# Kernel tuning notes

Measured on AMD Instinct MI355X. Metric: run time of the kernel, lower is better.

Reference implementation:

```python
import jax, jax.numpy as jnp
import numpy as np
from jax import lax

B, T, CIN, COUT, FACTOR = 2, 2048, 512, 512, 2
KUP = FACTOR * 2          # transposed-conv kernel
PUP = FACTOR // 2         # transposed-conv padding
KR, PR = 7, 3             # refine conv kernel/padding
EPS = 1e-5


def _ste(x, q):
    # straight-through estimator: forward = q, backward = identity
    return x + lax.stop_gradient(q - x)


def act_quant(x):
    # BitNet b1.58 per-token int8 absmax quant; x is (B, C, L), quant over C
    scale = 127.0 / jnp.maximum(jnp.max(jnp.abs(x), axis=1, keepdims=True), 1e-5)
    q = jnp.clip(jnp.round(x * scale), -128, 127) / scale
    return _ste(x, q)


def weight_quant(w):
    # ternary {-1,0,1} * scale, scale = mean |w|
    scale = 1.0 / jnp.maximum(jnp.mean(jnp.abs(w)), 1e-5)
    q = jnp.clip(jnp.round(w * scale), -1, 1) / scale
    return _ste(w, q)


def bit_conv1d(x, w, b, pad):
    # x: (B,C,L), w: (Cout,Cin,K) torch layout
    y = lax.conv_general_dilated(
        act_quant(x), weight_quant(w), window_strides=(1,),
        padding=[(pad, pad)], dimension_numbers=('NCH', 'OIH', 'NCH'))
    return y + b[None, :, None]


def bit_conv_transpose1d(x, w, b, stride, pad):
    # x: (B,Cin,L), w: (Cin,Cout,K) torch ConvTranspose1d layout
    k = w.shape[2]
    y = lax.conv_general_dilated(
        act_quant(x), jnp.flip(weight_quant(w), 2), window_strides=(1,),
        padding=[(k - 1 - pad, k - 1 - pad)], lhs_dilation=(stride,),
        dimension_numbers=('NCH', 'IOH', 'NCH'))
    return y + b[None, :, None]


def setup_inputs() -> dict:
    key = jax.random.key(0)
    ks = jax.random.split(key, 7)
    s_up = 1.0 / np.sqrt(CIN * KUP)
    s_r = 1.0 / np.sqrt(COUT * KR)
    return {
        'x': jax.random.normal(ks[0], (B, T, CIN), jnp.float32),
        'w_up': jax.random.normal(ks[1], (CIN, COUT, KUP), jnp.float32) * s_up,
        'b_up': jnp.zeros((COUT,), jnp.float32),
        'w_r1': jax.random.normal(ks[2], (COUT, COUT, KR), jnp.float32) * s_r,
        'b_r1': jnp.zeros((COUT,), jnp.float32),
        'w_r2': jax.random.normal(ks[3], (COUT, COUT, KR), jnp.float32) * s_r,
        'b_r2': jnp.zeros((COUT,), jnp.float32),
        'ln_w': jnp.ones((COUT,), jnp.float32),
        'ln_b': jnp.zeros((COUT,), jnp.float32),
    }


def reference(x, w_up, b_up, w_r1, b_r1, w_r2, b_r2, ln_w, ln_b):
    h = jnp.swapaxes(x, 1, 2)                                  # (B,Cin,T)
    h = bit_conv_transpose1d(h, w_up, b_up, FACTOR, PUP)       # (B,Cout,factor*T)
    r = bit_conv1d(h, w_r1, b_r1, PR)
    r = jax.nn.silu(r)
    r = bit_conv1d(r, w_r2, b_r2, PR)
    h = h + r
    h = jnp.swapaxes(h, 1, 2)                                  # (B,L,Cout)
    mu = jnp.mean(h, axis=-1, keepdims=True)
    var = jnp.mean(jnp.square(h - mu), axis=-1, keepdims=True)
    return (h - mu) * lax.rsqrt(var + EPS) * ln_w + ln_b
```

## Files before the change

kernel.cpp:

```cpp
#include <hip/hip_runtime.h>
#include <hip/hip_bf16.h>
#include <cstdint>
#include <cstddef>


#define B_ 2
#define T_ 2048
#define L_ 4096
#define C_ 512

static constexpr int NUP = 512 * 512 * 4;
static constexpr int NR  = 512 * 512 * 7;

using v4i  = __attribute__((ext_vector_type(4))) int;
using v16i = __attribute__((ext_vector_type(16))) int;

__device__ __forceinline__ void gl16(const void* g, void* l) {
  __builtin_amdgcn_global_load_lds((const __attribute__((address_space(1))) unsigned int*)g,
                                   (__attribute__((address_space(3))) unsigned int*)l,
                                   16, 0, 0);
}


__device__ inline float block_reduce_sum_256(float v) {
  #pragma unroll
  for (int off = 32; off > 0; off >>= 1) v += __shfl_down(v, off, 64);
  __shared__ float s[4];
  __syncthreads();
  if ((threadIdx.x & 63) == 0) s[threadIdx.x >> 6] = v;
  __syncthreads();
  return (s[0] + s[1]) + (s[2] + s[3]);
}

__global__ void abssum3_partial(const float* __restrict__ w0, const float* __restrict__ w1,
                                const float* __restrict__ w2, float* __restrict__ partial) {
  int y = blockIdx.y;
  const float* w = (y == 0) ? w0 : (y == 1) ? w1 : w2;
  int n = (y == 0) ? NUP : NR;
  int idx = blockIdx.x * 256 + threadIdx.x;
  float s = 0.f;
  for (int i = idx; i < n; i += gridDim.x * 256) s += fabsf(w[i]);
  s = block_reduce_sum_256(s);
  if (threadIdx.x == 0) partial[y * 256 + blockIdx.x] = s;
}

__global__ void abssum3_final(const float* __restrict__ partial, float* __restrict__ out) {
  int y = blockIdx.x;
  float v = partial[y * 256 + threadIdx.x];
  v = block_reduce_sum_256(v);
  if (threadIdx.x == 0) out[y] = v;
}

__global__ void tern_all_kernel(const float* __restrict__ wu, const float* __restrict__ w1,
                                const float* __restrict__ w2, int8_t* __restrict__ ou,
                                int8_t* __restrict__ o1, int8_t* __restrict__ o2,
                                const float* __restrict__ wsum) {
  int y = blockIdx.y;
  int idx = blockIdx.x * 256 + threadIdx.x;
  if (y == 0) {
    if (idx >= NUP) return;
    float mean = wsum[0] * (1.0f / (float)NUP);
    float scale = 1.0f / fmaxf(mean, 1e-5f);
    float t = rintf(wu[idx] * scale);
    t = fminf(fmaxf(t, -1.f), 1.f);
    int ci = idx >> 11;
    int co = (idx >> 2) & 511;
    int k = idx & 3;
    int ptap = (k == 3) ? 0 : (k == 1) ? 1 : (k == 2) ? 2 : 3;
    ou[(((size_t)ptap * 32 + (ci >> 4)) * 512 + co) * 16 + (ci & 15)] = (int8_t)t;
  } else {
    if (idx >= NR) return;
    const float* w = (y == 1) ? w1 : w2;
    int8_t* o = (y == 1) ? o1 : o2;
    float mean = wsum[y] * (1.0f / (float)NR);
    float scale = 1.0f / fmaxf(mean, 1e-5f);
    float t = rintf(w[idx] * scale);
    t = fminf(fmaxf(t, -1.f), 1.f);
    int co = idx / 3584;
    int rem = idx - co * 3584;
    int ci = rem / 7;
    int k = rem - ci * 7;
    o[(((size_t)k * 32 + (ci >> 4)) * 512 + co) * 16 + (ci & 15)] = (int8_t)t;
  }
}

__global__ void act_quant_kernel(const float* __restrict__ x, int8_t* __restrict__ qd,
                                 float* __restrict__ inv, int Lb, int lbsh, int LinH) {
  int tok = blockIdx.x;
  int b = tok >> lbsh;
  int t = tok & (Lb - 1);
  const float* row = x + (size_t)tok * C_;
  int tid = threadIdx.x;
  float v0 = row[tid];
  float v1 = row[tid + 256];
  float m = fmaxf(fabsf(v0), fabsf(v1));
  #pragma unroll
  for (int off = 32; off > 0; off >>= 1) m = fmaxf(m, __shfl_down(m, off, 64));
  __shared__ float s[4];
  __shared__ __align__(16) int8_t sq[512];
  if ((tid & 63) == 0) s[tid >> 6] = m;
  __syncthreads();
  m = fmaxf(fmaxf(s[0], s[1]), fmaxf(s[2], s[3]));
  float scale = 127.0f / fmaxf(m, 1e-5f);
  float q0 = fminf(fmaxf(rintf(v0 * scale), -128.f), 127.f);
  float q1 = fminf(fmaxf(rintf(v1 * scale), -128.f), 127.f);
  sq[tid] = (int8_t)q0;
  sq[tid + 256] = (int8_t)q1;
  __syncthreads();
  if (tid < 32)
    *(v4i*)(qd + ((size_t)(b * 32 + tid) * LinH + 8 + t) * 16) = *(const v4i*)(sq + tid * 16);
  if (tid == 0) inv[(size_t)b * LinH + 8 + t] = 1.0f / scale;
}

template<int NTAPS, bool CONVT>
__global__ __launch_bounds__(512, 4)
void conv_mfma(const int8_t* __restrict__ qin, const float* __restrict__ invp, int LinH,
               const int8_t* __restrict__ wq, const float* __restrict__ wsum, int widx,
               float wninv, const float* __restrict__ bias, const float* __restrict__ res,
               float* __restrict__ outp, int Lout, int do_silu) {
  __shared__ __align__(16) int8_t sA[32 * 38 * 16];
  __shared__ float sInv[40];

  const int tid = threadIdx.x;
  const int w = tid >> 6, lane = tid & 63, q = lane >> 5, l31 = lane & 31;
  const int n0 = (blockIdx.x & 1) * 256;
  const int t0 = (blockIdx.x >> 1) * 32;
  const int b = blockIdx.y;
  int s0 = -3;
  const int8_t* wq_p = wq;
  float* out_b = outp + (size_t)b * Lout * 512;
  int rstride = 512;
  if (CONVT) {
    int parity = blockIdx.z;
    s0 = parity - 1;
    wq_p += (size_t)parity * 2 * 32 * 512 * 16;
    out_b += parity * 512;
    rstride = 1024;
  }
  const int8_t* qin_b = qin + (size_t)b * 32 * LinH * 16;
  const float* inv_b = invp + (size_t)b * LinH + 8;

  #pragma unroll
  for (int i = 0; i < 3; ++i) {
    int base = i * 512 + w * 64;
    if (base < 1216) {
      int u = base + lane;
      int kq = u / 38;
      int row = u - kq * 38;
      gl16(qin_b + ((size_t)kq * LinH + (size_t)(t0 + 5 + row)) * 16,
           sA + (size_t)base * 16);
    }
  }
  if (tid < 38) sInv[tid] = inv_b[t0 - 3 + tid];
  __syncthreads();

  float fs[16];
  v16i accA{}, accB{};
  #pragma unroll
  for (int r = 0; r < 16; ++r) { fs[r] = 0.f; accA[r] = 0; accB[r] = 0; }

  const int col = n0 + w * 32 + l31;
  const int8_t* wt_base = wq_p + ((size_t)q * 512 + (size_t)col) * 16;

  #pragma unroll 1
  for (int tap = 0; tap < NTAPS; ++tap) {
    const int shift = s0 + tap;
    const int8_t* aP = sA + (((size_t)q * 38) + (size_t)(3 + shift + l31)) * 16;
    const int8_t* wt = wt_base + (size_t)tap * (32 * 512 * 16);
    #pragma unroll
    for (int ks = 0; ks < 16; ks += 2) {
      v4i a0 = *(const v4i*)(aP + (size_t)ks * (2 * 38 * 16));
      v4i b0 = *(const v4i*)(wt + (size_t)ks * 16384);
      accA = __builtin_amdgcn_mfma_i32_32x32x32_i8(a0, b0, accA, 0, 0, 0);
      v4i a1 = *(const v4i*)(aP + (size_t)(ks + 1) * (2 * 38 * 16));
      v4i b1 = *(const v4i*)(wt + (size_t)(ks + 1) * 16384);
      accB = __builtin_amdgcn_mfma_i32_32x32x32_i8(a1, b1, accB, 0, 0, 0);
    }
    #pragma unroll
    for (int r = 0; r < 16; ++r) {
      int ro = (r & 3) + 8 * (r >> 2) + 4 * q;
      float sc = sInv[3 + shift + ro];
      fs[r] = fmaf((float)(accA[r] + accB[r]), sc, fs[r]);
      accA[r] = 0; accB[r] = 0;
    }
  }

  float wdq = fmaxf(wsum[widx] * wninv, 1e-5f);
  float bv = bias[col];
  #pragma unroll
  for (int r = 0; r < 16; ++r) {
    int row = t0 + (r & 3) + 8 * (r >> 2) + 4 * q;
    float y = fs[r] * wdq + bv;
    if (do_silu) y = y / (1.0f + expf(-y));
    if (res) y += res[((size_t)b * Lout + row) * 512 + col];
    out_b[(size_t)row * rstride + col] = y;
  }
}

__global__ void ln_kernel(const float* __restrict__ x, const float* __restrict__ g,
                          const float* __restrict__ be, float* __restrict__ out) {
  int tok = blockIdx.x;
  const float* row = x + (size_t)tok * C_;
  int tid = threadIdx.x;
  float v0 = row[tid];
  float v1 = row[tid + 256];
  float total = block_reduce_sum_256(v0 + v1);
  float mu = total * (1.0f / (float)C_);
  float d0 = v0 - mu, d1 = v1 - mu;
  float vs = block_reduce_sum_256(d0 * d0 + d1 * d1);
  float var = vs * (1.0f / (float)C_);
  float r = 1.0f / sqrtf(var + 1e-5f);
  size_t base = (size_t)tok * C_;
  out[base + tid] = d0 * r * g[tid] + be[tid];
  out[base + tid + 256] = d1 * r * g[tid + 256] + be[tid + 256];
}


extern "C" void kernel_launch(void* const* d_in, const int* in_sizes, int n_in,
                              void* d_out, int out_size, void* d_ws, size_t ws_size,
                              hipStream_t stream) {
  const float* x    = (const float*)d_in[0];
  const float* w_up = (const float*)d_in[1];
  const float* b_up = (const float*)d_in[2];
  const float* w_r1 = (const float*)d_in[3];
  const float* b_r1 = (const float*)d_in[4];
  const float* w_r2 = (const float*)d_in[5];
  const float* b_r2 = (const float*)d_in[6];
  const float* ln_w = (const float*)d_in[7];
  const float* ln_b = (const float*)d_in[8];
  float* out = (float*)d_out;

  const int LXH = T_ + 16;
  const int LHH = L_ + 16;

  char* ws = (char*)d_ws;
  size_t off = 0;
  auto alloc = [&](size_t sz) { size_t p = off; off += (sz + 255) & ~(size_t)255; return p; };
  float*  wsum = (float*) (ws + alloc(256));
  int8_t* qx   = (int8_t*)(ws + alloc((size_t)B_ * 32 * LXH * 16));
  int8_t* qh   = (int8_t*)(ws + alloc((size_t)B_ * 32 * LHH * 16));
  float*  invx = (float*) (ws + alloc((size_t)B_ * LXH * 4));
  float*  invh = (float*) (ws + alloc((size_t)B_ * LHH * 4));
  size_t zero_bytes = off;
  float*  partial = (float*)(ws + alloc(3 * 256 * 4));
  int8_t* wqup = (int8_t*)(ws + alloc((size_t)4 * 32 * 512 * 16));
  int8_t* wq1  = (int8_t*)(ws + alloc((size_t)7 * 32 * 512 * 16));
  int8_t* wq2  = (int8_t*)(ws + alloc((size_t)7 * 32 * 512 * 16));
  float*  h    = (float*) (ws + alloc((size_t)B_ * L_ * C_ * 4));
  float*  r    = (float*) (ws + alloc((size_t)B_ * L_ * C_ * 4));

  hipMemsetAsync(ws, 0, zero_bytes, stream);

  abssum3_partial<<<dim3(256, 3), 256, 0, stream>>>(w_up, w_r1, w_r2, partial);
  abssum3_final<<<3, 256, 0, stream>>>(partial, wsum);
  tern_all_kernel<<<dim3(NR / 256, 3), 256, 0, stream>>>(w_up, w_r1, w_r2,
                                                         wqup, wq1, wq2, wsum);

  act_quant_kernel<<<B_ * T_, 256, 0, stream>>>(x, qx, invx, T_, 11, LXH);

  conv_mfma<2, true><<<dim3(2 * 64, B_, 2), 512, 0, stream>>>(
      qx, invx, LXH, wqup, wsum, 0, 1.0f / (float)NUP, b_up, nullptr, h, L_, 0);

  act_quant_kernel<<<B_ * L_, 256, 0, stream>>>(h, qh, invh, L_, 12, LHH);

  conv_mfma<7, false><<<dim3(2 * 128, B_, 1), 512, 0, stream>>>(
      qh, invh, LHH, wq1, wsum, 1, 1.0f / (float)NR, b_r1, nullptr, r, L_, 1);

  act_quant_kernel<<<B_ * L_, 256, 0, stream>>>(r, qh, invh, L_, 12, LHH);

  conv_mfma<7, false><<<dim3(2 * 128, B_, 1), 512, 0, stream>>>(
      qh, invh, LHH, wq2, wsum, 2, 1.0f / (float)NR, b_r2, h, r, L_, 0);

  ln_kernel<<<B_ * L_, 256, 0, stream>>>(r, ln_w, ln_b, out);
}
```

Measured before the change: 207.4 us.

## Fuse act-quant and layernorm epilogues into conv kernels with full-width N tiles

Each conv block now computes all 512 output channels for its 32 tokens, with each wave doing two MFMAs per A fragment. This lets per-token reductions happen in the epilogue: the per-token int8 quantization of the next conv's input, and the final residual add plus LayerNorm. That removes three standalone act_quant/LN kernels and the fp32 intermediate round-trips of r. In exchange the grids are half as large, occupancy drops (launch bounds 4→2, extra LDS), and the epilogues add block-wide syncs.

Result: slower. 227.8 us (+9.8%).

```diff
diff --git a/kernel.cpp b/kernel.cpp
--- a/kernel.cpp
+++ b/kernel.cpp
@@ -112,30 +112,34 @@
   if (tid == 0) inv[(size_t)b * LinH + 8 + t] = 1.0f / scale;
 }
 
-template<int NTAPS, bool CONVT>
-__global__ __launch_bounds__(512, 4)
-void conv_mfma(const int8_t* __restrict__ qin, const float* __restrict__ invp, int LinH,
-               const int8_t* __restrict__ wq, const float* __restrict__ wsum, int widx,
-               float wninv, const float* __restrict__ bias, const float* __restrict__ res,
-               float* __restrict__ outp, int Lout, int do_silu) {
+template<int NTAPS, bool CONVT, int EPI>
+__global__ __launch_bounds__(512, 2)
+void conv_fused(const int8_t* __restrict__ qin, const float* __restrict__ invp, int LinH,
+                const int8_t* __restrict__ wq, const float* __restrict__ wsum, int widx,
+                float wninv, const float* __restrict__ bias,
+                float* __restrict__ hout,
+                int8_t* __restrict__ qout, float* __restrict__ invout, int LoutH,
+                const float* __restrict__ res, const float* __restrict__ g,
+                const float* __restrict__ be, float* __restrict__ lnout, int Lout) {
   __shared__ __align__(16) int8_t sA[32 * 38 * 16];
   __shared__ float sInv[40];
+  __shared__ float sRedA[8][32];
+  __shared__ float sRedB[8][32];
+  __shared__ float sS0[32];
+  __shared__ float sS1[32];
+  __shared__ __align__(16) int8_t sQ[32][512];
 
   const int tid = threadIdx.x;
   const int w = tid >> 6, lane = tid & 63, q = lane >> 5, l31 = lane & 31;
-  const int n0 = (blockIdx.x & 1) * 256;
-  const int t0 = (blockIdx.x >> 1) * 32;
+  const int t0 = blockIdx.x * 32;
   const int b = blockIdx.y;
   int s0 = -3;
   const int8_t* wq_p = wq;
-  float* out_b = outp + (size_t)b * Lout * 512;
-  int rstride = 512;
+  int parity = 0;
   if (CONVT) {
-    int parity = blockIdx.z;
+    parity = blockIdx.z;
     s0 = parity - 1;
     wq_p += (size_t)parity * 2 * 32 * 512 * 16;
-    out_b += parity * 512;
-    rstride = 1024;
   }
   const int8_t* qin_b = qin + (size_t)b * 32 * LinH * 16;
   const float* inv_b = invp + (size_t)b * LinH + 8;
@@ -154,13 +158,13 @@
   if (tid < 38) sInv[tid] = inv_b[t0 - 3 + tid];
   __syncthreads();
 
-  float fs[16];
-  v16i accA{}, accB{};
-  #pragma unroll
-  for (int r = 0; r < 16; ++r) { fs[r] = 0.f; accA[r] = 0; accB[r] = 0; }
-
-  const int col = n0 + w * 32 + l31;
-  const int8_t* wt_base = wq_p + ((size_t)q * 512 + (size_t)col) * 16;
+  float fs0[16], fs1[16];
+  v16i acc0{}, acc1{};
+  #pragma unroll
+  for (int r = 0; r < 16; ++r) { fs0[r] = 0.f; fs1[r] = 0.f; acc0[r] = 0; acc1[r] = 0; }
+
+  const int col0 = w * 64 + l31;
+  const int8_t* wt_base = wq_p + ((size_t)q * 512 + (size_t)col0) * 16;
 
   #pragma unroll 1
   for (int tap = 0; tap < NTAPS; ++tap) {
@@ -168,51 +172,140 @@
     const int8_t* aP = sA + (((size_t)q * 38) + (size_t)(3 + shift + l31)) * 16;
     const int8_t* wt = wt_base + (size_t)tap * (32 * 512 * 16);
     #pragma unroll
-    for (int ks = 0; ks < 16; ks += 2) {
-      v4i a0 = *(const v4i*)(aP + (size_t)ks * (2 * 38 * 16));
+    for (int ks = 0; ks < 16; ++ks) {
+      v4i a  = *(const v4i*)(aP + (size_t)ks * (2 * 38 * 16));
       v4i b0 = *(const v4i*)(wt + (size_t)ks * 16384);
-      accA = __builtin_amdgcn_mfma_i32_32x32x32_i8(a0, b0, accA, 0, 0, 0);
-      v4i a1 = *(const v4i*)(aP + (size_t)(ks + 1) * (2 * 38 * 16));
-      v4i b1 = *(const v4i*)(wt + (size_t)(ks + 1) * 16384);
-      accB = __builtin_amdgcn_mfma_i32_32x32x32_i8(a1, b1, accB, 0, 0, 0);
+      v4i b1 = *(const v4i*)(wt + (size_t)ks * 16384 + 512);
+      acc0 = __builtin_amdgcn_mfma_i32_32x32x32_i8(a, b0, acc0, 0, 0, 0);
+      acc1 = __builtin_amdgcn_mfma_i32_32x32x32_i8(a, b1, acc1, 0, 0, 0);
     }
     #pragma unroll
     for (int r = 0; r < 16; ++r) {
       int ro = (r & 3) + 8 * (r >> 2) + 4 * q;
       float sc = sInv[3 + shift + ro];
-      fs[r] = fmaf((float)(accA[r] + accB[r]), sc, fs[r]);
-      accA[r] = 0; accB[r] = 0;
-    }
-  }
-
-  float wdq = fmaxf(wsum[widx] * wninv, 1e-5f);
-  float bv = bias[col];
+      fs0[r] = fmaf((float)acc0[r], sc, fs0[r]);
+      fs1[r] = fmaf((float)acc1[r], sc, fs1[r]);
+      acc0[r] = 0; acc1[r] = 0;
+    }
+  }
+
+  const float wdq = fmaxf(wsum[widx] * wninv, 1e-5f);
+  const float bv0 = bias[col0], bv1 = bias[col0 + 32];
   #pragma unroll
   for (int r = 0; r < 16; ++r) {
-    int row = t0 + (r & 3) + 8 * (r >> 2) + 4 * q;
-    float y = fs[r] * wdq + bv;
-    if (do_silu) y = y / (1.0f + expf(-y));
-    if (res) y += res[((size_t)b * Lout + row) * 512 + col];
-    out_b[(size_t)row * rstride + col] = y;
-  }
-}
-
-__global__ void ln_kernel(const float* __restrict__ x, const float* __restrict__ g,
-                          const float* __restrict__ be, float* __restrict__ out) {
-  int tok = blockIdx.x;
-  const float* row = x + (size_t)tok * C_;
-  int tid = threadIdx.x;
-  float v0 = row[tid];
-  float v1 = row[tid + 256];
-  float total = block_reduce_sum_256(v0 + v1);
-  float mu = total * (1.0f / (float)C_);
-  float d0 = v0 - mu, d1 = v1 - mu;
-  float vs = block_reduce_sum_256(d0 * d0 + d1 * d1);
-  float var = vs * (1.0f / (float)C_);
-  float r = 1.0f / sqrtf(var + 1e-5f);
-  size_t base = (size_t)tok * C_;
-  out[base + tid] = d0 * r * g[tid] + be[tid];
-  out[base + tid + 256] = d1 * r * g[tid + 256] + be[tid + 256];
+    fs0[r] = fs0[r] * wdq + bv0;
+    fs1[r] = fs1[r] * wdq + bv1;
+  }
+
+  if constexpr (EPI == 0) {
+    #pragma unroll
+    for (int r = 0; r < 16; ++r) {
+      int ro = (r & 3) + 8 * (r >> 2) + 4 * q;
+      size_t base = ((size_t)b * Lout + 2 * (size_t)(t0 + ro) + parity) * 512;
+      hout[base + col0] = fs0[r];
+      hout[base + col0 + 32] = fs1[r];
+    }
+  }
+  if constexpr (EPI == 1) {
+    #pragma unroll
+    for (int r = 0; r < 16; ++r) {
+      fs0[r] = fs0[r] / (1.0f + expf(-fs0[r]));
+      fs1[r] = fs1[r] / (1.0f + expf(-fs1[r]));
+    }
+  }
+
+  if constexpr (EPI <= 1) {
+    #pragma unroll
+    for (int r = 0; r < 16; ++r) {
+      int ro = (r & 3) + 8 * (r >> 2) + 4 * q;
+      float m = fmaxf(fabsf(fs0[r]), fabsf(fs1[r]));
+      #pragma unroll
+      for (int off = 16; off > 0; off >>= 1) m = fmaxf(m, __shfl_xor(m, off, 64));
+      if (l31 == 0) sRedA[w][ro] = m;
+    }
+    __syncthreads();
+    if (tid < 32) {
+      float m = sRedA[0][tid];
+      #pragma unroll
+      for (int ww = 1; ww < 8; ++ww) m = fmaxf(m, sRedA[ww][tid]);
+      float mm = fmaxf(m, 1e-5f);
+      sS0[tid] = 127.0f / mm;
+      int tok = CONVT ? (2 * (t0 + tid) + parity) : (t0 + tid);
+      invout[(size_t)b * LoutH + 8 + tok] = mm * (1.0f / 127.0f);
+    }
+    __syncthreads();
+    #pragma unroll
+    for (int r = 0; r < 16; ++r) {
+      int ro = (r & 3) + 8 * (r >> 2) + 4 * q;
+      float sc = sS0[ro];
+      float q0 = fminf(fmaxf(rintf(fs0[r] * sc), -128.f), 127.f);
+      float q1 = fminf(fmaxf(rintf(fs1[r] * sc), -128.f), 127.f);
+      sQ[ro][col0] = (int8_t)q0;
+      sQ[ro][col0 + 32] = (int8_t)q1;
+    }
+    __syncthreads();
+    #pragma unroll
+    for (int it = 0; it < 2; ++it) {
+      int u = it * 512 + tid;
+      int row = u >> 5, unit = u & 31;
+      int tok = CONVT ? (2 * (t0 + row) + parity) : (t0 + row);
+      *(v4i*)(qout + (((size_t)b * 32 + unit) * LoutH + 8 + tok) * 16) =
+          *(const v4i*)(&sQ[row][unit * 16]);
+    }
+  } else {
+    #pragma unroll
+    for (int r = 0; r < 16; ++r) {
+      int ro = (r & 3) + 8 * (r >> 2) + 4 * q;
+      size_t base = ((size_t)b * Lout + (size_t)(t0 + ro)) * 512;
+      fs0[r] += res[base + col0];
+      fs1[r] += res[base + col0 + 32];
+    }
+    #pragma unroll
+    for (int r = 0; r < 16; ++r) {
+      int ro = (r & 3) + 8 * (r >> 2) + 4 * q;
+      float s = fs0[r] + fs1[r];
+      #pragma unroll
+      for (int off = 16; off > 0; off >>= 1) s += __shfl_xor(s, off, 64);
+      if (l31 == 0) sRedA[w][ro] = s;
+    }
+    __syncthreads();
+    if (tid < 32) {
+      float s = sRedA[0][tid];
+      #pragma unroll
+      for (int ww = 1; ww < 8; ++ww) s += sRedA[ww][tid];
+      sS0[tid] = s * (1.0f / 512.0f);
+    }
+    __syncthreads();
+    #pragma unroll
+    for (int r = 0; r < 16; ++r) {
+      int ro = (r & 3) + 8 * (r >> 2) + 4 * q;
+      float mu = sS0[ro];
+      float d0 = fs0[r] - mu, d1 = fs1[r] - mu;
+      float ss = d0 * d0 + d1 * d1;
+      #pragma unroll
+      for (int off = 16; off > 0; off >>= 1) ss += __shfl_xor(ss, off, 64);
+      if (l31 == 0) sRedB[w][ro] = ss;
+    }
+    __syncthreads();
+    if (tid < 32) {
+      float ssum = sRedB[0][tid];
+      #pragma unroll
+      for (int ww = 1; ww < 8; ++ww) ssum += sRedB[ww][tid];
+      float var = ssum * (1.0f / 512.0f);
+      sS1[tid] = 1.0f / sqrtf(var + 1e-5f);
+    }
+    __syncthreads();
+    const float g0 = g[col0], g1 = g[col0 + 32];
+    const float e0 = be[col0], e1 = be[col0 + 32];
+    #pragma unroll
+    for (int r = 0; r < 16; ++r) {
+      int ro = (r & 3) + 8 * (r >> 2) + 4 * q;
+      float mu = sS0[ro], rs = sS1[ro];
+      size_t base = ((size_t)b * Lout + (size_t)(t0 + ro)) * 512;
+      lnout[base + col0]      = (fs0[r] - mu) * rs * g0 + e0;
+      lnout[base + col0 + 32] = (fs1[r] - mu) * rs * g1 + e1;
+    }
+  }
 }
 
 
@@ -236,18 +329,19 @@
   char* ws = (char*)d_ws;
   size_t off = 0;
   auto alloc = [&](size_t sz) { size_t p = off; off += (sz + 255) & ~(size_t)255; return p; };
-  float*  wsum = (float*) (ws + alloc(256));
-  int8_t* qx   = (int8_t*)(ws + alloc((size_t)B_ * 32 * LXH * 16));
-  int8_t* qh   = (int8_t*)(ws + alloc((size_t)B_ * 32 * LHH * 16));
-  float*  invx = (float*) (ws + alloc((size_t)B_ * LXH * 4));
-  float*  invh = (float*) (ws + alloc((size_t)B_ * LHH * 4));
+  float*  wsum  = (float*) (ws + alloc(256));
+  int8_t* qx    = (int8_t*)(ws + alloc((size_t)B_ * 32 * LXH * 16));
+  int8_t* qh    = (int8_t*)(ws + alloc((size_t)B_ * 32 * LHH * 16));
+  int8_t* qh2   = (int8_t*)(ws + alloc((size_t)B_ * 32 * LHH * 16));
+  float*  invx  = (float*) (ws + alloc((size_t)B_ * LXH * 4));
+  float*  invh  = (float*) (ws + alloc((size_t)B_ * LHH * 4));
+  float*  invh2 = (float*) (ws + alloc((size_t)B_ * LHH * 4));
   size_t zero_bytes = off;
   float*  partial = (float*)(ws + alloc(3 * 256 * 4));
   int8_t* wqup = (int8_t*)(ws + alloc((size_t)4 * 32 * 512 * 16));
   int8_t* wq1  = (int8_t*)(ws + alloc((size_t)7 * 32 * 512 * 16));
   int8_t* wq2  = (int8_t*)(ws + alloc((size_t)7 * 32 * 512 * 16));
   float*  h    = (float*) (ws + alloc((size_t)B_ * L_ * C_ * 4));
-  float*  r    = (float*) (ws + alloc((size_t)B_ * L_ * C_ * 4));
 
   hipMemsetAsync(ws, 0, zero_bytes, stream);
 
@@ -258,18 +352,15 @@
 
   act_quant_kernel<<<B_ * T_, 256, 0, stream>>>(x, qx, invx, T_, 11, LXH);
 
-  conv_mfma<2, true><<<dim3(2 * 64, B_, 2), 512, 0, stream>>>(
-      qx, invx, LXH, wqup, wsum, 0, 1.0f / (float)NUP, b_up, nullptr, h, L_, 0);
-
-  act_quant_kernel<<<B_ * L_, 256, 0, stream>>>(h, qh, invh, L_, 12, LHH);
-
-  conv_mfma<7, false><<<dim3(2 * 128, B_, 1), 512, 0, stream>>>(
-      qh, invh, LHH, wq1, wsum, 1, 1.0f / (float)NR, b_r1, nullptr, r, L_, 1);
-
-  act_quant_kernel<<<B_ * L_, 256, 0, stream>>>(r, qh, invh, L_, 12, LHH);
-
-  conv_mfma<7, false><<<dim3(2 * 128, B_, 1), 512, 0, stream>>>(
-      qh, invh, LHH, wq2, wsum, 2, 1.0f / (float)NR, b_r2, h, r, L_, 0);
-
-  ln_kernel<<<B_ * L_, 256, 0, stream>>>(r, ln_w, ln_b, out);
-}
+  conv_fused<2, true, 0><<<dim3(64, B_, 2), 512, 0, stream>>>(
+      qx, invx, LXH, wqup, wsum, 0, 1.0f / (float)NUP, b_up,
+      h, qh, invh, LHH, nullptr, nullptr, nullptr, nullptr, L_);
+
+  conv_fused<7, false, 1><<<dim3(128, B_, 1), 512, 0, stream>>>(
+      qh, invh, LHH, wq1, wsum, 1, 1.0f / (float)NR, b_r1,
+      nullptr, qh2, invh2, LHH, nullptr, nullptr, nullptr, nullptr, L_);
+
+  conv_fused<7, false, 2><<<dim3(128, B_, 1), 512, 0, stream>>>(
+      qh2, invh2, LHH, wq2, wsum, 2, 1.0f / (float)NR, b_r2,
+      nullptr, nullptr, nullptr, 0, h, ln_w, ln_b, out, L_);
+}
```
